# Optimization experiments

Hardware: AMD Instinct MI355X
Metric: run time of the kernel (lower is better)

The kernel has to match this reference:

```python
import jax, jax.numpy as jnp
import numpy as np

KD, KY, KX = 3, 3, 3  # kernel_size from init_kwargs


def setup_inputs() -> dict:
    key = jax.random.key(0)
    x = jax.random.normal(key, (4, 2, 64, 256, 256), dtype=jnp.float32)
    return {"x": x}


def reference(x):
    # x: [B, CH, D, H, W]
    B, CH, D, H, W = x.shape
    pd, py, px = (KD - 1) // 2, (KY - 1) // 2, (KX - 1) // 2
    # replicate padding (torch F.pad mode='replicate' == jnp.pad mode='edge')
    xp = jnp.pad(x, ((0, 0), (0, 0), (pd, pd), (py, py), (px, px)), mode='edge')
    center = (KD * KY * KX) // 2  # flattened center position, excluded from max
    # running max over the 26 non-center neighbors; never materializes the
    # [B, CH, 27, D, H, W] tensor the torch conv3d path creates.
    max_nc = jnp.full(x.shape, -jnp.inf, dtype=x.dtype)
    idx = 0
    for i in range(KD):
        for j in range(KY):
            for k in range(KX):
                if idx != center:
                    shifted = xp[:, :, i:i + D, j:j + H, k:k + W]
                    max_nc = jnp.maximum(max_nc, shifted)
                idx += 1
    mask = x > max_nc  # strict local maximum (excluding self)
    return x * mask.astype(x.dtype)
```

## Files before the change

kernel.cpp:

```cpp
#include <hip/hip_runtime.h>


constexpr int D_   = 64;
constexpr int H_   = 256;
constexpr int W_   = 256;
constexpr int HW_  = H_ * W_;
constexpr int NVOL = 8;
constexpr int DC   = 8;

__device__ __forceinline__ float f3(float a, float b, float c) {
    return fmaxf(fmaxf(a, b), c);
}

__global__ __launch_bounds__(256, 4)
void nms3d(const float* __restrict__ x, float* __restrict__ out)
{
    const int tx = threadIdx.x;
    const int ty = threadIdx.y;
    const int h  = (blockIdx.y << 2) + ty;
    const int n  = blockIdx.z;
    const int z0 = blockIdx.x * DC;

    const float* __restrict__ base  = x   + (size_t)n * D_ * HW_;
    float* __restrict__       obase = out + (size_t)n * D_ * HW_;

    const int r0 = (h == 0)      ? 0      : h - 1;
    const int r2 = (h == H_ - 1) ? H_ - 1 : h + 1;
    const int c  = tx << 2;

    const float* spA = base + (size_t)max(z0 - 1, 0) * HW_;
    const float* spB = base + (size_t)z0 * HW_;
    float4 a0 = *(const float4*)(spA + r0 * W_ + c);
    float4 b0 = *(const float4*)(spA + h  * W_ + c);
    float4 d0 = *(const float4*)(spA + r2 * W_ + c);
    float4 a1 = *(const float4*)(spB + r0 * W_ + c);
    float4 b1 = *(const float4*)(spB + h  * W_ + c);
    float4 d1 = *(const float4*)(spB + r2 * W_ + c);

    float4 vm9_pp = {0,0,0,0};
    float4 vm9_p  = {0,0,0,0};
    float4 cr8_p  = {0,0,0,0};
    float4 vprev  = {0,0,0,0};

#pragma unroll
    for (int t = 0; t < DC + 2; ++t) {
        const int zi = z0 - 1 + t;

        const int zn = min(zi + 2, D_ - 1);
        const float* spn = base + (size_t)zn * HW_;
        const float4 a2 = *(const float4*)(spn + r0 * W_ + c);
        const float4 b2 = *(const float4*)(spn + h  * W_ + c);
        const float4 d2 = *(const float4*)(spn + r2 * W_ + c);

        float4 va;
        va.x = fmaxf(a0.x, d0.x); va.y = fmaxf(a0.y, d0.y);
        va.z = fmaxf(a0.z, d0.z); va.w = fmaxf(a0.w, d0.w);

        float vaL = __shfl_up(va.w, 1);   if (tx == 0)  vaL = va.x;
        float vaR = __shfl_down(va.x, 1); if (tx == 63) vaR = va.w;
        float bL  = __shfl_up(b0.w, 1);   if (tx == 0)  bL  = b0.x;
        float bR  = __shfl_down(b0.x, 1); if (tx == 63) bR  = b0.w;

        float4 hv;
        hv.x = f3(vaL, va.x, va.y);  hv.y = f3(va.x, va.y, va.z);
        hv.z = f3(va.y, va.z, va.w); hv.w = f3(va.z, va.w, vaR);
        float4 nb;
        nb.x = fmaxf(bL, b0.y);  nb.y = fmaxf(b0.x, b0.z);
        nb.z = fmaxf(b0.y, b0.w); nb.w = fmaxf(b0.z, bR);

        float4 c8, cur;
        c8.x  = fmaxf(hv.x, nb.x); c8.y  = fmaxf(hv.y, nb.y);
        c8.z  = fmaxf(hv.z, nb.z); c8.w  = fmaxf(hv.w, nb.w);
        cur.x = fmaxf(c8.x, b0.x); cur.y = fmaxf(c8.y, b0.y);
        cur.z = fmaxf(c8.z, b0.z); cur.w = fmaxf(c8.w, b0.w);

        if (zi > z0) {
            float4 mx, o;
            mx.x = f3(vm9_pp.x, cr8_p.x, cur.x);
            mx.y = f3(vm9_pp.y, cr8_p.y, cur.y);
            mx.z = f3(vm9_pp.z, cr8_p.z, cur.z);
            mx.w = f3(vm9_pp.w, cr8_p.w, cur.w);
            o.x = vprev.x > mx.x ? vprev.x : 0.0f;
            o.y = vprev.y > mx.y ? vprev.y : 0.0f;
            o.z = vprev.z > mx.z ? vprev.z : 0.0f;
            o.w = vprev.w > mx.w ? vprev.w : 0.0f;
            *(float4*)(obase + (size_t)(zi - 1) * HW_ + (size_t)h * W_ + c) = o;
        }
        vm9_pp = vm9_p; vm9_p = cur; cr8_p = c8; vprev = b0;
        a0 = a1; b0 = b1; d0 = d1;
        a1 = a2; b1 = b2; d1 = d2;
    }
}

extern "C" void kernel_launch(void* const* d_in, const int* in_sizes, int n_in,
                              void* d_out, int out_size, void* d_ws, size_t ws_size,
                              hipStream_t stream)
{
    const float* x = (const float*)d_in[0];
    float* out = (float*)d_out;
    dim3 block(64, 4, 1);
    dim3 grid(D_ / DC, H_ / 4, NVOL);
    nms3d<<<grid, block, 0, stream>>>(x, out);
}
```

Measured before the change: 228.1 us.

## Stage depth planes in double-buffered LDS to share H-halo rows across threads

Each block now covers 8 rows instead of 4. Every depth plane of the tile, plus one halo row above and below, is loaded into a double-buffered shared-memory array. Threads read their up, center and down rows from LDS instead of each issuing three global loads per plane, which cuts redundant global/L2 traffic from 3x to about 1.25x. The cost is a __syncthreads per depth step, extra LDS traffic, and 20KB of shared memory per block, which may limit occupancy.

New measurement: 231.6 us. No clear change (+1.6%).

```diff
diff --git a/kernel.cpp b/kernel.cpp
--- a/kernel.cpp
+++ b/kernel.cpp
@@ -7,35 +7,42 @@
 constexpr int HW_  = H_ * W_;
 constexpr int NVOL = 8;
 constexpr int DC   = 8;
+constexpr int ROWS = 8;
+constexpr int SROWS = ROWS + 2;
 
 __device__ __forceinline__ float f3(float a, float b, float c) {
     return fmaxf(fmaxf(a, b), c);
 }
 
-__global__ __launch_bounds__(256, 4)
+__global__ __launch_bounds__(512, 4)
 void nms3d(const float* __restrict__ x, float* __restrict__ out)
 {
+    __shared__ float buf[2][SROWS][W_];
+
     const int tx = threadIdx.x;
     const int ty = threadIdx.y;
-    const int h  = (blockIdx.y << 2) + ty;
+    const int h0 = blockIdx.y * ROWS;
+    const int h  = h0 + ty;
     const int n  = blockIdx.z;
     const int z0 = blockIdx.x * DC;
+    const int c  = tx << 2;
 
     const float* __restrict__ base  = x   + (size_t)n * D_ * HW_;
     float* __restrict__       obase = out + (size_t)n * D_ * HW_;
 
-    const int r0 = (h == 0)      ? 0      : h - 1;
-    const int r2 = (h == H_ - 1) ? H_ - 1 : h + 1;
-    const int c  = tx << 2;
+    const int extra = (ty == 0) ? 0 : (ty == ROWS - 1 ? SROWS - 1 : -1);
+    const int gx = (extra == 0) ? max(h0 - 1, 0) : min(h0 + ROWS, H_ - 1);
 
-    const float* spA = base + (size_t)max(z0 - 1, 0) * HW_;
-    const float* spB = base + (size_t)z0 * HW_;
-    float4 a0 = *(const float4*)(spA + r0 * W_ + c);
-    float4 b0 = *(const float4*)(spA + h  * W_ + c);
-    float4 d0 = *(const float4*)(spA + r2 * W_ + c);
-    float4 a1 = *(const float4*)(spB + r0 * W_ + c);
-    float4 b1 = *(const float4*)(spB + h  * W_ + c);
-    float4 d1 = *(const float4*)(spB + r2 * W_ + c);
+    {
+        const float* sp = base + (size_t)max(z0 - 1, 0) * HW_;
+        const float4 r = *(const float4*)(sp + h * W_ + c);
+        *(float4*)&buf[0][ty + 1][c] = r;
+        if (extra >= 0) {
+            const float4 rx = *(const float4*)(sp + gx * W_ + c);
+            *(float4*)&buf[0][extra][c] = rx;
+        }
+    }
+    __syncthreads();
 
     float4 vm9_pp = {0,0,0,0};
     float4 vm9_p  = {0,0,0,0};
@@ -44,51 +51,62 @@
 
 #pragma unroll
     for (int t = 0; t < DC + 2; ++t) {
-        const int zi = z0 - 1 + t;
+        const int zi  = z0 - 1 + t;
+        const int cur = t & 1, nxt = cur ^ 1;
 
-        const int zn = min(zi + 2, D_ - 1);
-        const float* spn = base + (size_t)zn * HW_;
-        const float4 a2 = *(const float4*)(spn + r0 * W_ + c);
-        const float4 b2 = *(const float4*)(spn + h  * W_ + c);
-        const float4 d2 = *(const float4*)(spn + r2 * W_ + c);
+        float4 r, rx;
+        const bool do_stage = (t < DC + 1);
+        if (do_stage) {
+            const float* sp = base + (size_t)min(zi + 1, D_ - 1) * HW_;
+            r = *(const float4*)(sp + h * W_ + c);
+            if (extra >= 0) rx = *(const float4*)(sp + gx * W_ + c);
+        }
+
+        const float4 a = *(const float4*)&buf[cur][ty    ][c];
+        const float4 b = *(const float4*)&buf[cur][ty + 1][c];
+        const float4 d = *(const float4*)&buf[cur][ty + 2][c];
 
         float4 va;
-        va.x = fmaxf(a0.x, d0.x); va.y = fmaxf(a0.y, d0.y);
-        va.z = fmaxf(a0.z, d0.z); va.w = fmaxf(a0.w, d0.w);
+        va.x = fmaxf(a.x, d.x); va.y = fmaxf(a.y, d.y);
+        va.z = fmaxf(a.z, d.z); va.w = fmaxf(a.w, d.w);
 
         float vaL = __shfl_up(va.w, 1);   if (tx == 0)  vaL = va.x;
         float vaR = __shfl_down(va.x, 1); if (tx == 63) vaR = va.w;
-        float bL  = __shfl_up(b0.w, 1);   if (tx == 0)  bL  = b0.x;
-        float bR  = __shfl_down(b0.x, 1); if (tx == 63) bR  = b0.w;
+        float bL  = __shfl_up(b.w, 1);    if (tx == 0)  bL  = b.x;
+        float bR  = __shfl_down(b.x, 1);  if (tx == 63) bR  = b.w;
 
         float4 hv;
         hv.x = f3(vaL, va.x, va.y);  hv.y = f3(va.x, va.y, va.z);
         hv.z = f3(va.y, va.z, va.w); hv.w = f3(va.z, va.w, vaR);
         float4 nb;
-        nb.x = fmaxf(bL, b0.y);  nb.y = fmaxf(b0.x, b0.z);
-        nb.z = fmaxf(b0.y, b0.w); nb.w = fmaxf(b0.z, bR);
+        nb.x = fmaxf(bL, b.y);   nb.y = fmaxf(b.x, b.z);
+        nb.z = fmaxf(b.y, b.w);  nb.w = fmaxf(b.z, bR);
 
-        float4 c8, cur;
-        c8.x  = fmaxf(hv.x, nb.x); c8.y  = fmaxf(hv.y, nb.y);
-        c8.z  = fmaxf(hv.z, nb.z); c8.w  = fmaxf(hv.w, nb.w);
-        cur.x = fmaxf(c8.x, b0.x); cur.y = fmaxf(c8.y, b0.y);
-        cur.z = fmaxf(c8.z, b0.z); cur.w = fmaxf(c8.w, b0.w);
+        float4 c8, cu;
+        c8.x = fmaxf(hv.x, nb.x); c8.y = fmaxf(hv.y, nb.y);
+        c8.z = fmaxf(hv.z, nb.z); c8.w = fmaxf(hv.w, nb.w);
+        cu.x = fmaxf(c8.x, b.x);  cu.y = fmaxf(c8.y, b.y);
+        cu.z = fmaxf(c8.z, b.z);  cu.w = fmaxf(c8.w, b.w);
 
         if (zi > z0) {
             float4 mx, o;
-            mx.x = f3(vm9_pp.x, cr8_p.x, cur.x);
-            mx.y = f3(vm9_pp.y, cr8_p.y, cur.y);
-            mx.z = f3(vm9_pp.z, cr8_p.z, cur.z);
-            mx.w = f3(vm9_pp.w, cr8_p.w, cur.w);
+            mx.x = f3(vm9_pp.x, cr8_p.x, cu.x);
+            mx.y = f3(vm9_pp.y, cr8_p.y, cu.y);
+            mx.z = f3(vm9_pp.z, cr8_p.z, cu.z);
+            mx.w = f3(vm9_pp.w, cr8_p.w, cu.w);
             o.x = vprev.x > mx.x ? vprev.x : 0.0f;
             o.y = vprev.y > mx.y ? vprev.y : 0.0f;
             o.z = vprev.z > mx.z ? vprev.z : 0.0f;
             o.w = vprev.w > mx.w ? vprev.w : 0.0f;
             *(float4*)(obase + (size_t)(zi - 1) * HW_ + (size_t)h * W_ + c) = o;
         }
-        vm9_pp = vm9_p; vm9_p = cur; cr8_p = c8; vprev = b0;
-        a0 = a1; b0 = b1; d0 = d1;
-        a1 = a2; b1 = b2; d1 = d2;
+        vm9_pp = vm9_p; vm9_p = cu; cr8_p = c8; vprev = b;
+
+        if (do_stage) {
+            *(float4*)&buf[nxt][ty + 1][c] = r;
+            if (extra >= 0) *(float4*)&buf[nxt][extra][c] = rx;
+        }
+        __syncthreads();
     }
 }
 
@@ -98,7 +116,7 @@
 {
     const float* x = (const float*)d_in[0];
     float* out = (float*)d_out;
-    dim3 block(64, 4, 1);
-    dim3 grid(D_ / DC, H_ / 4, NVOL);
+    dim3 block(64, ROWS, 1);
+    dim3 grid(D_ / DC, H_ / ROWS, NVOL);
     nms3d<<<grid, block, 0, stream>>>(x, out);
 }
```
